# Kernel optimization log

Measured on AMD Instinct MI355X. Metric: run time of the kernel, lower is better.

## Reference

```python
import jax, jax.numpy as jnp
import numpy as np

# Production-scale dims
B, S, D = 8, 2048, 1024          # batch, seq_len, d_model
E, ES, V = 32, 128, 1024         # n_experts, expert_size, v_dim (= d_model)
K = 4                            # top-k experts per token (n_heads)


def setup_inputs() -> dict:
    key = jax.random.key(0)
    k1, k2, k3, k4 = jax.random.split(key, 4)
    return {
        "x": jax.random.normal(k1, (B, S, D), jnp.float32),
        "keys": jax.random.normal(k2, (E, D, ES), jnp.float32) * (D ** -0.5),
        "values": jax.random.normal(k3, (E, ES, V), jnp.float32) * (ES ** -0.5),
        "expert_sel": jax.random.normal(k4, (E, D), jnp.float32) * (D ** -0.5),
    }


def reference(x, keys, values, expert_sel):
    """SigmaMoELayer forward (eval mode, sigmoid selection, no bias/dropout).
    Returns (out [B,S,V], reg_loss scalar)."""
    n_experts = expert_sel.shape[0]
    # Router logits: [B, S, E]
    sel_raw = jnp.einsum('bsd,ed->bse', x, expert_sel)

    # Entropy regularization: log_softmax over experts, log-mean over all tokens
    l = jax.nn.log_softmax(sel_raw.reshape(-1, n_experts), axis=-1)   # [T, E]
    lm = jax.scipy.special.logsumexp(l, axis=0) - jnp.log(jnp.asarray(l.shape[0], l.dtype))
    reg_loss = jnp.sum(lm * jnp.exp(lm))  # == -entropy_l(lm).mean()

    # Sigmoid gating + top-k expert selection
    sel = jax.nn.sigmoid(sel_raw)
    sel_val, sel_idx = jax.lax.top_k(sel, K)                          # [B,S,K]

    # Scatter gate values onto the expert axis: gate[b,s,e] = sel_val if e selected else 0
    gate = jnp.einsum('bske,bsk->bse',
                      jax.nn.one_hot(sel_idx, n_experts, dtype=x.dtype), sel_val)

    # Expert up-projection + ReLU, gated (relu(mask*z) == mask*relu(z), experts distinct)
    h = jax.nn.relu(jnp.einsum('bsd,edf->bsef', x, keys)) * gate[..., None]  # [B,S,E,ES]
    # Expert down-projection + combine across experts
    out = jnp.einsum('bsef,efv->bsv', h, values)                      # [B,S,V]
    return out, reg_loss
```

## Files before the change

kernel.cpp:

```cpp
#include <hip/hip_runtime.h>

typedef unsigned int uint;
typedef unsigned short ushort;

#define TT 16384
#define DD 1024
#define EE 32
#define ESS 128
#define VV 1024
#define KK 4
#define TILE 64
#define NTILE_MAX 1056
#define RSPLIT 8

typedef __attribute__((ext_vector_type(8))) short bf16x8;
typedef __attribute__((ext_vector_type(16))) float f32x16;

#define WS_SELRAW   0
#define WS_GATES    524288
#define WS_PGATE    589824
#define WS_STATS    655360
#define WS_LMSUMS   655360
#define WS_COUNTS   655392
#define WS_OFFSETS  655424
#define WS_CURSORS  655457
#define WS_NTILES   655489
#define WS_TMAPE    655490
#define WS_TMAPT    656546
#define WS_IDXS     657602
#define WS_PERM     723138
#define WS_XB       788736
#define WS_KF       9177344
#define WS_VF       11274496
#define WS_ISLOT    13371648
#define WS_STG      13437184
#define WS_NEED_U   46991616ull

__device__ __forceinline__ ushort f2b(float f) {
    uint u = __builtin_bit_cast(uint, f);
    u = (u + 0x7fffu + ((u >> 16) & 1u)) >> 16;
    return (ushort)u;
}
__device__ __forceinline__ uint bpack(float lo, float hi) {
    return (uint)f2b(lo) | ((uint)f2b(hi) << 16);
}
__device__ __forceinline__ float b2f(ushort b) {
    uint u = (uint)b << 16;
    return __builtin_bit_cast(float, u);
}

__device__ __forceinline__ void gload_lds16(const void* g, void* l) {
    __builtin_amdgcn_global_load_lds(
        (const __attribute__((address_space(1))) uint*)g,
        (__attribute__((address_space(3))) uint*)l, 16, 0, 0);
}

__global__ __launch_bounds__(256) void k_prep_k(const float* __restrict__ keys,
                                                ushort* __restrict__ kfb) {
    const int e = blockIdx.x >> 6, ks = blockIdx.x & 63;
    const int nf = threadIdx.x >> 6, l = threadIdx.x & 63;
    const int f = nf * 32 + (l & 31);
    const int d0 = ks * 16 + (l >> 5) * 8;
    const float* src = keys + ((size_t)e * DD + d0) * ESS + f;
    float v[8];
#pragma unroll
    for (int j = 0; j < 8; j++) v[j] = src[(size_t)j * ESS];
    uint4 r = { bpack(v[0], v[1]), bpack(v[2], v[3]), bpack(v[4], v[5]), bpack(v[6], v[7]) };
    const size_t off = (((size_t)e * 64 + ks) * 4 + nf) * 512 + l * 8;
    *(uint4*)(kfb + off) = r;
}

__global__ __launch_bounds__(512) void k_prep_v(const float* __restrict__ values,
                                                ushort* __restrict__ vfb) {
    const int e = blockIdx.x >> 5, nv = blockIdx.x & 31;
    const int ks = threadIdx.x >> 6, l = threadIdx.x & 63;
    const int v0 = nv * 32 + (l & 31);
    const int f0 = ks * 16 + (l >> 5) * 8;
    const float* src = values + ((size_t)e * ESS + f0) * VV + v0;
    float v[8];
#pragma unroll
    for (int j = 0; j < 8; j++) v[j] = src[(size_t)j * VV];
    uint4 r = { bpack(v[0], v[1]), bpack(v[2], v[3]), bpack(v[4], v[5]), bpack(v[6], v[7]) };
    const size_t off = (((size_t)e * 32 + nv) * 8 + ks) * 512 + l * 8;
    *(uint4*)(vfb + off) = r;
}

__global__ __launch_bounds__(256) void k_router(const float* __restrict__ x,
                                                const float* __restrict__ sel,
                                                float* __restrict__ sel_part,
                                                uint* __restrict__ xbu) {
    __shared__ float xs[64][68];
    __shared__ float ss[32][68];
    const int tid = threadIdx.x;
    const int t0 = blockIdx.x * 64;
    const int dch = blockIdx.y;
    const int el = tid & 31;
    const int tg = tid >> 5;
    float acc[8];
#pragma unroll
    for (int i = 0; i < 8; i++) acc[i] = 0.f;

    const int dlen = DD / RSPLIT;
    for (int dc = dch * dlen; dc < dch * dlen + dlen; dc += 64) {
#pragma unroll
        for (int i = 0; i < 4; i++) {
            int q = tid + 256 * i;
            int r = q >> 4, c4 = q & 15;
            size_t gi = (size_t)(t0 + r) * DD + dc + c4 * 4;
            float4 v = *(const float4*)&x[gi];
            *(float4*)&xs[r][c4 * 4] = v;
            uint2 bv = { bpack(v.x, v.y), bpack(v.z, v.w) };
            *(uint2*)&xbu[gi / 2] = bv;
        }
#pragma unroll
        for (int i = 0; i < 2; i++) {
            int q = tid + 256 * i;
            int e = q >> 4, c4 = q & 15;
            float4 v = *(const float4*)&sel[(size_t)e * DD + dc + c4 * 4];
            *(float4*)&ss[e][c4 * 4] = v;
        }
        __syncthreads();
#pragma unroll
        for (int d4 = 0; d4 < 16; d4++) {
            float4 sv = *(const float4*)&ss[el][d4 * 4];
#pragma unroll
            for (int i = 0; i < 8; i++) {
                float4 xv = *(const float4*)&xs[tg * 8 + i][d4 * 4];
                acc[i] += xv.x * sv.x + xv.y * sv.y + xv.z * sv.z + xv.w * sv.w;
            }
        }
        __syncthreads();
    }
    float* dst = sel_part + (size_t)dch * TT * EE;
#pragma unroll
    for (int i = 0; i < 8; i++)
        dst[(size_t)(t0 + tg * 8 + i) * EE + el] = acc[i];
}

__global__ __launch_bounds__(256) void k_token(const float* __restrict__ sel_part,
                                               float* __restrict__ gates,
                                               int* __restrict__ idxs,
                                               float* __restrict__ lm_sums,
                                               int* __restrict__ counts) {
    __shared__ int hist[EE];
    __shared__ float lmh[EE];
    const int tid = threadIdx.x;
    if (tid < EE) { hist[tid] = 0; lmh[tid] = 0.f; }
    __syncthreads();

    const int t = blockIdx.x * 256 + tid;
    float v[32];
#pragma unroll
    for (int j = 0; j < 8; j++) {
        float4 q[RSPLIT];
#pragma unroll
        for (int p = 0; p < RSPLIT; p++)
            q[p] = *(const float4*)&sel_part[((size_t)p * TT + t) * EE + j * 4];
        v[j * 4 + 0] = ((q[0].x + q[1].x) + (q[2].x + q[3].x)) + ((q[4].x + q[5].x) + (q[6].x + q[7].x));
        v[j * 4 + 1] = ((q[0].y + q[1].y) + (q[2].y + q[3].y)) + ((q[4].y + q[5].y) + (q[6].y + q[7].y));
        v[j * 4 + 2] = ((q[0].z + q[1].z) + (q[2].z + q[3].z)) + ((q[4].z + q[5].z) + (q[6].z + q[7].z));
        v[j * 4 + 3] = ((q[0].w + q[1].w) + (q[2].w + q[3].w)) + ((q[4].w + q[5].w) + (q[6].w + q[7].w));
    }
    float m = v[0];
#pragma unroll
    for (int e = 1; e < 32; e++) m = fmaxf(m, v[e]);
    float s = 0.f;
#pragma unroll
    for (int e = 0; e < 32; e++) s += expf(v[e] - m);
    const float lse = logf(s) + m;

    float sg[32];
#pragma unroll
    for (int e = 0; e < 32; e++) sg[e] = 1.f / (1.f + expf(-v[e]));

    unsigned taken = 0u;
#pragma unroll
    for (int k = 0; k < KK; k++) {
        float best = -1.f; int bi = 0;
#pragma unroll
        for (int e = 0; e < 32; e++) {
            bool free_e = !((taken >> e) & 1u);
            if (free_e && sg[e] > best) { best = sg[e]; bi = e; }
        }
        taken |= 1u << bi;
        gates[t * KK + k] = best;
        idxs[t * KK + k] = bi;
        atomicAdd(&hist[bi], 1);
    }

#pragma unroll
    for (int e = 0; e < 32; e++) {
        float pv = expf(v[e] - lse);
#pragma unroll
        for (int o = 32; o >= 1; o >>= 1) pv += __shfl_xor(pv, o, 64);
        if ((tid & 63) == 0) atomicAdd(&lmh[e], pv);
    }
    __syncthreads();
    if (tid < EE) {
        atomicAdd(&counts[tid], hist[tid]);
        atomicAdd(&lm_sums[tid], lmh[tid]);
    }
}

__global__ void k_scan(const int* __restrict__ counts, int* __restrict__ offsets,
                       int* __restrict__ cursors, int* __restrict__ tmape,
                       int* __restrict__ tmapt, int* __restrict__ ntiles,
                       const float* __restrict__ lm_sums, float* __restrict__ out_reg) {
    const int lane = threadIdx.x;
    int c = (lane < EE) ? counts[lane] : 0;
    int p = c;
#pragma unroll
    for (int o = 1; o < 32; o <<= 1) { int u = __shfl_up(p, o, 64); if (lane >= o) p += u; }
    const int off = p - c;
    if (lane < EE) { offsets[lane] = off; cursors[lane] = off; }
    if (lane == EE - 1) offsets[EE] = p;

    int nt = (c + TILE - 1) / TILE;
    int q = nt;
#pragma unroll
    for (int o = 1; o < 32; o <<= 1) { int u = __shfl_up(q, o, 64); if (lane >= o) q += u; }
    const int tb = q - nt;
    if (lane < EE)
        for (int j = 0; j < nt; j++) { tmape[tb + j] = lane; tmapt[tb + j] = j; }
    if (lane == EE - 1) ntiles[0] = q;

    float rv = 0.f;
    if (lane < EE) {
        float pe = lm_sums[lane] * (1.f / (float)TT);
        rv = pe * logf(pe);
    }
#pragma unroll
    for (int o = 16; o >= 1; o >>= 1) rv += __shfl_down(rv, o, 64);
    if (lane == 0) out_reg[0] = rv;
}

__global__ __launch_bounds__(256) void k_scatter(const int* __restrict__ idxs,
                                                 const float* __restrict__ gates,
                                                 int* __restrict__ cursors,
                                                 int* __restrict__ perm,
                                                 float* __restrict__ pgate,
                                                 int* __restrict__ islot) {
    __shared__ int lh[EE];
    __shared__ int lbase[EE];
    const int tid = threadIdx.x;
    if (tid < EE) lh[tid] = 0;
    __syncthreads();
    const int t = blockIdx.x * 256 + tid;
    int ee[KK], rk[KK];
#pragma unroll
    for (int k = 0; k < KK; k++) {
        ee[k] = idxs[t * KK + k];
        rk[k] = atomicAdd(&lh[ee[k]], 1);
    }
    __syncthreads();
    if (tid < EE) lbase[tid] = atomicAdd(&cursors[tid], lh[tid]);
    __syncthreads();
#pragma unroll
    for (int k = 0; k < KK; k++) {
        int pos = lbase[ee[k]] + rk[k];
        perm[pos] = t;
        pgate[pos] = gates[t * KK + k];
        islot[t * KK + k] = pos;
    }
}

template <bool STG>
__global__ __launch_bounds__(256, 3) void k_expert(
    const ushort* __restrict__ xb, const ushort* __restrict__ kfb,
    const ushort* __restrict__ vfb,
    const int* __restrict__ perm, const float* __restrict__ pgate,
    const int* __restrict__ offsets, const int* __restrict__ counts,
    const int* __restrict__ tmape, const int* __restrict__ tmapt,
    const int* __restrict__ ntiles, ushort* __restrict__ stg,
    float* __restrict__ out)
{
    __shared__ __align__(1024) char xsb[2][64 * 256];
    __shared__ __align__(16) ushort hs[64][128];
    __shared__ float gl[64];
    __shared__ int tl[64];

    const int bid = (blockIdx.x & 7) * 132 + (blockIdx.x >> 3);
    if (bid >= ntiles[0]) return;
    const int e = tmape[bid];
    const int base = offsets[e] + tmapt[bid] * TILE;
    const int nr = min(TILE, offsets[e] + counts[e] - base);
    const int tid = threadIdx.x;

    if (tid < 64) {
        int tok = 0; float g = 0.f;
        if (tid < nr) { tok = perm[base + tid]; g = pgate[base + tid]; }
        tl[tid] = tok; gl[tid] = g;
    }
    __syncthreads();

    const int lane = tid & 63, wid = tid >> 6;
    const int wm = wid >> 1, wn = wid & 1;
    const int l31 = lane & 31, l5 = lane >> 5;

    const char* xbytes = (const char*)xb;
    const ushort* kb = kfb + ((size_t)e * 256 + wn * 2) * 512 + lane * 8;

    int srow[4]; const char* ssrc[4];
#pragma unroll
    for (int i = 0; i < 4; i++) {
        srow[i] = wid * 4096 + i * 1024;
        int row = wid * 16 + i * 4 + (lane >> 4);
        int colb = (lane & 15) * 16;
        ssrc[i] = xbytes + (size_t)tl[row] * 2048 + (colb ^ ((row & 15) << 4));
    }

    f32x16 acc0, acc1;
#pragma unroll
    for (int r = 0; r < 16; r++) { acc0[r] = 0.f; acc1[r] = 0.f; }

#pragma unroll
    for (int i = 0; i < 4; i++)
        gload_lds16(ssrc[i], xsb[0] + srow[i]);

    bf16x8 b0p[8], b1p[8];
#pragma unroll
    for (int j = 0; j < 8; j++) {
        b0p[j] = *(const bf16x8*)(kb + (size_t)j * 2048);
        b1p[j] = *(const bf16x8*)(kb + (size_t)j * 2048 + 512);
    }
    asm volatile("s_waitcnt vmcnt(16)" ::: "memory");
    __builtin_amdgcn_s_barrier();
    __builtin_amdgcn_sched_barrier(0);

    const int hr = wm * 32 + l31;
    const int asw = (hr & 15) << 4;

    for (int c = 0; c < 8; c++) {
        const int cur = c & 1;
        if (c < 7) {
#pragma unroll
            for (int i = 0; i < 4; i++)
                gload_lds16(ssrc[i] + (c + 1) * 256, xsb[cur ^ 1] + srow[i]);
        }
        const char* xcur = xsb[cur];
#pragma unroll
        for (int ksl = 0; ksl < 8; ksl++) {
            bf16x8 a = *(const bf16x8*)(xcur + hr * 256 + ((ksl * 32 + l5 * 16) ^ asw));
            int ks = c * 8 + ksl;
            acc0 = __builtin_amdgcn_mfma_f32_32x32x16_bf16(a, b0p[ksl], acc0, 0, 0, 0);
            acc1 = __builtin_amdgcn_mfma_f32_32x32x16_bf16(a, b1p[ksl], acc1, 0, 0, 0);
            int nk = (ks + 8) & 63;
            b0p[ksl] = *(const bf16x8*)(kb + (size_t)nk * 2048);
            b1p[ksl] = *(const bf16x8*)(kb + (size_t)nk * 2048 + 512);
        }
        asm volatile("s_waitcnt vmcnt(16)" ::: "memory");
        __builtin_amdgcn_s_barrier();
        __builtin_amdgcn_sched_barrier(0);
    }

#pragma unroll
    for (int r = 0; r < 16; r++) {
        int row = (r & 3) + 8 * (r >> 2) + 4 * l5;
        int grow = wm * 32 + row;
        float g = gl[grow];
        int c0 = wn * 64 + l31;
        int c1 = c0 + 32;
        int sw = (grow & 7) << 3;
        hs[grow][c0 ^ sw] = f2b(fmaxf(acc0[r], 0.f) * g);
        hs[grow][c1 ^ sw] = f2b(fmaxf(acc1[r], 0.f) * g);
    }
    __syncthreads();

    bf16x8 af[8];
    const int hsw = (hr & 7) << 3;
#pragma unroll
    for (int ks = 0; ks < 8; ks++) {
        int cc = ks * 16 + l5 * 8;
        af[ks] = *(const bf16x8*)&hs[hr][cc ^ hsw];
    }

    const ushort* vb = vfb + ((size_t)e * 32 + wn * 16) * 4096 + lane * 8;
    bf16x8 vpa[4], vpb[4];
#pragma unroll
    for (int j = 0; j < 4; j++) {
        vpa[j] = *(const bf16x8*)(vb + (size_t)j * 512);
        vpb[j] = *(const bf16x8*)(vb + (size_t)(4 + j) * 512);
    }

#pragma unroll
    for (int nv = 0; nv < 16; nv++) {
        f32x16 acc;
#pragma unroll
        for (int r = 0; r < 16; r++) acc[r] = 0.f;
#pragma unroll
        for (int ks = 0; ks < 4; ks++)
            acc = __builtin_amdgcn_mfma_f32_32x32x16_bf16(af[ks], vpa[ks], acc, 0, 0, 0);
        if (nv < 15) {
#pragma unroll
            for (int j = 0; j < 4; j++)
                vpa[j] = *(const bf16x8*)(vb + ((size_t)(nv + 1) * 8 + j) * 512);
        }
#pragma unroll
        for (int ks = 0; ks < 4; ks++)
            acc = __builtin_amdgcn_mfma_f32_32x32x16_bf16(af[4 + ks], vpb[ks], acc, 0, 0, 0);
        if (nv < 15) {
#pragma unroll
            for (int j = 0; j < 4; j++)
                vpb[j] = *(const bf16x8*)(vb + ((size_t)(nv + 1) * 8 + 4 + j) * 512);
        }
        const int colb = wn * 512 + nv * 32 + l31;
#pragma unroll
        for (int r = 0; r < 16; r++) {
            int row = wm * 32 + (r & 3) + 8 * (r >> 2) + 4 * l5;
            if (row < nr) {
                if (STG)
                    stg[(size_t)(base + row) * VV + colb] = f2b(acc[r]);
                else
                    atomicAdd(&out[(size_t)tl[row] * VV + colb], acc[r]);
            }
        }
    }
}

__global__ __launch_bounds__(256) void k_combine(const ushort* __restrict__ stg,
                                                 const int* __restrict__ islot,
                                                 float* __restrict__ out) {
    const int tid = threadIdx.x;
    const int t = blockIdx.x * 2 + (tid >> 7);
    const int c8 = (tid & 127) * 8;
    const int4 sl = *(const int4*)&islot[t * KK];
    float acc[8];
#pragma unroll
    for (int j = 0; j < 8; j++) acc[j] = 0.f;
    const int slots[4] = { sl.x, sl.y, sl.z, sl.w };
#pragma unroll
    for (int k = 0; k < KK; k++) {
        bf16x8 v = *(const bf16x8*)(stg + (size_t)slots[k] * VV + c8);
#pragma unroll
        for (int j = 0; j < 8; j++) acc[j] += b2f((ushort)v[j]);
    }
    float4 o0 = { acc[0], acc[1], acc[2], acc[3] };
    float4 o1 = { acc[4], acc[5], acc[6], acc[7] };
    *(float4*)&out[(size_t)t * VV + c8] = o0;
    *(float4*)&out[(size_t)t * VV + c8 + 4] = o1;
}

extern "C" void kernel_launch(void* const* d_in, const int* in_sizes, int n_in,
                              void* d_out, int out_size, void* d_ws, size_t ws_size,
                              hipStream_t stream) {
    const float* x      = (const float*)d_in[0];
    const float* keys   = (const float*)d_in[1];
    const float* values = (const float*)d_in[2];
    const float* esel   = (const float*)d_in[3];
    float* out = (float*)d_out;

    float* wsf = (float*)d_ws;
    int*   wsi = (int*)d_ws;

    float* gates   = wsf + WS_GATES;
    float* pgate   = wsf + WS_PGATE;
    float* lm_sums = wsf + WS_LMSUMS;
    int*   counts  = wsi + WS_COUNTS;
    int*   offsets = wsi + WS_OFFSETS;
    int*   cursors = wsi + WS_CURSORS;
    int*   ntiles  = wsi + WS_NTILES;
    int*   tmape   = wsi + WS_TMAPE;
    int*   tmapt   = wsi + WS_TMAPT;
    int*   idxs    = wsi + WS_IDXS;
    int*   perm    = wsi + WS_PERM;
    int*   islot   = wsi + WS_ISLOT;
    uint*   xbu = (uint*)(wsf + WS_XB);
    ushort* xb  = (ushort*)xbu;
    ushort* kfb = (ushort*)(wsf + WS_KF);
    ushort* vfb = (ushort*)(wsf + WS_VF);
    ushort* stg = (ushort*)(wsf + WS_STG);

    const bool use_stg = ws_size >= WS_NEED_U * 4ull;
    float* sel_part = use_stg ? (float*)stg : (float*)kfb;

    if (!use_stg)
        hipMemsetAsync(d_out, 0, (size_t)TT * VV * sizeof(float), stream);
    hipMemsetAsync(wsf + WS_STATS, 0, 64 * sizeof(float), stream);

    k_router<<<dim3(TT / 64, RSPLIT), 256, 0, stream>>>(x, esel, sel_part, xbu);
    k_token<<<TT / 256, 256, 0, stream>>>(sel_part, gates, idxs, lm_sums, counts);

    k_prep_k<<<EE * 64, 256, 0, stream>>>(keys, kfb);
    k_prep_v<<<EE * 32, 512, 0, stream>>>(values, vfb);

    k_scan<<<1, 64, 0, stream>>>(counts, offsets, cursors, tmape, tmapt, ntiles,
                                 lm_sums, out + (size_t)TT * VV);
    k_scatter<<<TT / 256, 256, 0, stream>>>(idxs, gates, cursors, perm, pgate, islot);
    if (use_stg) {
        k_expert<true><<<NTILE_MAX, 256, 0, stream>>>(xb, kfb, vfb, perm, pgate,
                                                      offsets, counts, tmape, tmapt,
                                                      ntiles, stg, out);
        k_combine<<<TT / 2, 256, 0, stream>>>(stg, islot, out);
    } else {
        k_expert<false><<<NTILE_MAX, 256, 0, stream>>>(xb, kfb, vfb, perm, pgate,
                                                       offsets, counts, tmape, tmapt,
                                                       ntiles, stg, out);
    }
}
```

Measured before the change: 212.3 us.

## Repartition expert GEMM waves to split only along N, reusing B fragments across M

Each of the four waves previously owned a 32-row by 64-column quadrant of the 64x128 hidden tile and of the output. Now each wave covers all 64 token rows and a quarter of the columns, in both the up-projection and the down-projection. Every key and value fragment loaded from global memory now feeds two MFMAs (one per 32-row half), which halves per-wave weight traffic and prefetch register use. In exchange, each wave makes twice as many LDS reads of activation rows.

Result: slower. 278.3 us (+31.1%).

```diff
diff --git a/kernel.cpp b/kernel.cpp
--- a/kernel.cpp
+++ b/kernel.cpp
@@ -294,11 +294,11 @@
     __syncthreads();
 
     const int lane = tid & 63, wid = tid >> 6;
-    const int wm = wid >> 1, wn = wid & 1;
+    const int wn = wid;
     const int l31 = lane & 31, l5 = lane >> 5;
 
     const char* xbytes = (const char*)xb;
-    const ushort* kb = kfb + ((size_t)e * 256 + wn * 2) * 512 + lane * 8;
+    const ushort* kb = kfb + ((size_t)e * 256 + wn) * 512 + lane * 8;
 
     int srow[4]; const char* ssrc[4];
 #pragma unroll
@@ -317,18 +317,15 @@
     for (int i = 0; i < 4; i++)
         gload_lds16(ssrc[i], xsb[0] + srow[i]);
 
-    bf16x8 b0p[8], b1p[8];
-#pragma unroll
-    for (int j = 0; j < 8; j++) {
-        b0p[j] = *(const bf16x8*)(kb + (size_t)j * 2048);
-        b1p[j] = *(const bf16x8*)(kb + (size_t)j * 2048 + 512);
-    }
-    asm volatile("s_waitcnt vmcnt(16)" ::: "memory");
+    bf16x8 bp[8];
+#pragma unroll
+    for (int j = 0; j < 8; j++)
+        bp[j] = *(const bf16x8*)(kb + (size_t)j * 2048);
+    asm volatile("s_waitcnt vmcnt(8)" ::: "memory");
     __builtin_amdgcn_s_barrier();
     __builtin_amdgcn_sched_barrier(0);
 
-    const int hr = wm * 32 + l31;
-    const int asw = (hr & 15) << 4;
+    const int asw = (l31 & 15) << 4;
 
     for (int c = 0; c < 8; c++) {
         const int cur = c & 1;
@@ -340,78 +337,71 @@
         const char* xcur = xsb[cur];
 #pragma unroll
         for (int ksl = 0; ksl < 8; ksl++) {
-            bf16x8 a = *(const bf16x8*)(xcur + hr * 256 + ((ksl * 32 + l5 * 16) ^ asw));
+            int co = (ksl * 32 + l5 * 16) ^ asw;
+            bf16x8 a0 = *(const bf16x8*)(xcur + l31 * 256 + co);
+            bf16x8 a1 = *(const bf16x8*)(xcur + (32 + l31) * 256 + co);
             int ks = c * 8 + ksl;
-            acc0 = __builtin_amdgcn_mfma_f32_32x32x16_bf16(a, b0p[ksl], acc0, 0, 0, 0);
-            acc1 = __builtin_amdgcn_mfma_f32_32x32x16_bf16(a, b1p[ksl], acc1, 0, 0, 0);
+            acc0 = __builtin_amdgcn_mfma_f32_32x32x16_bf16(a0, bp[ksl], acc0, 0, 0, 0);
+            acc1 = __builtin_amdgcn_mfma_f32_32x32x16_bf16(a1, bp[ksl], acc1, 0, 0, 0);
             int nk = (ks + 8) & 63;
-            b0p[ksl] = *(const bf16x8*)(kb + (size_t)nk * 2048);
-            b1p[ksl] = *(const bf16x8*)(kb + (size_t)nk * 2048 + 512);
-        }
-        asm volatile("s_waitcnt vmcnt(16)" ::: "memory");
+            bp[ksl] = *(const bf16x8*)(kb + (size_t)nk * 2048);
+        }
+        asm volatile("s_waitcnt vmcnt(8)" ::: "memory");
         __builtin_amdgcn_s_barrier();
         __builtin_amdgcn_sched_barrier(0);
     }
 
 #pragma unroll
     for (int r = 0; r < 16; r++) {
-        int row = (r & 3) + 8 * (r >> 2) + 4 * l5;
-        int grow = wm * 32 + row;
-        float g = gl[grow];
-        int c0 = wn * 64 + l31;
-        int c1 = c0 + 32;
-        int sw = (grow & 7) << 3;
-        hs[grow][c0 ^ sw] = f2b(fmaxf(acc0[r], 0.f) * g);
-        hs[grow][c1 ^ sw] = f2b(fmaxf(acc1[r], 0.f) * g);
-    }
-    __syncthreads();
-
-    bf16x8 af[8];
-    const int hsw = (hr & 7) << 3;
-#pragma unroll
-    for (int ks = 0; ks < 8; ks++) {
-        int cc = ks * 16 + l5 * 8;
-        af[ks] = *(const bf16x8*)&hs[hr][cc ^ hsw];
-    }
-
-    const ushort* vb = vfb + ((size_t)e * 32 + wn * 16) * 4096 + lane * 8;
-    bf16x8 vpa[4], vpb[4];
-#pragma unroll
-    for (int j = 0; j < 4; j++) {
-        vpa[j] = *(const bf16x8*)(vb + (size_t)j * 512);
-        vpb[j] = *(const bf16x8*)(vb + (size_t)(4 + j) * 512);
-    }
-
-#pragma unroll
-    for (int nv = 0; nv < 16; nv++) {
-        f32x16 acc;
-#pragma unroll
-        for (int r = 0; r < 16; r++) acc[r] = 0.f;
-#pragma unroll
-        for (int ks = 0; ks < 4; ks++)
-            acc = __builtin_amdgcn_mfma_f32_32x32x16_bf16(af[ks], vpa[ks], acc, 0, 0, 0);
-        if (nv < 15) {
-#pragma unroll
-            for (int j = 0; j < 4; j++)
-                vpa[j] = *(const bf16x8*)(vb + ((size_t)(nv + 1) * 8 + j) * 512);
-        }
-#pragma unroll
-        for (int ks = 0; ks < 4; ks++)
-            acc = __builtin_amdgcn_mfma_f32_32x32x16_bf16(af[4 + ks], vpb[ks], acc, 0, 0, 0);
-        if (nv < 15) {
-#pragma unroll
-            for (int j = 0; j < 4; j++)
-                vpb[j] = *(const bf16x8*)(vb + ((size_t)(nv + 1) * 8 + 4 + j) * 512);
-        }
-        const int colb = wn * 512 + nv * 32 + l31;
+        int row0 = (r & 3) + 8 * (r >> 2) + 4 * l5;
+        int row1 = row0 + 32;
+        int cc = wn * 32 + l31;
+        hs[row0][cc ^ ((row0 & 7) << 3)] = f2b(fmaxf(acc0[r], 0.f) * gl[row0]);
+        hs[row1][cc ^ ((row1 & 7) << 3)] = f2b(fmaxf(acc1[r], 0.f) * gl[row1]);
+    }
+    __syncthreads();
+
+    bf16x8 af[2][8];
+#pragma unroll
+    for (int b = 0; b < 2; b++) {
+        int hr2 = b * 32 + l31;
+        int hsw = (hr2 & 7) << 3;
+#pragma unroll
+        for (int ks = 0; ks < 8; ks++)
+            af[b][ks] = *(const bf16x8*)&hs[hr2][(ks * 16 + l5 * 8) ^ hsw];
+    }
+
+    const ushort* vb = vfb + ((size_t)e * 32 + wn * 8) * 4096 + lane * 8;
+    bf16x8 vp[8];
+#pragma unroll
+    for (int ks = 0; ks < 8; ks++)
+        vp[ks] = *(const bf16x8*)(vb + (size_t)ks * 512);
+
+#pragma unroll
+    for (int j = 0; j < 8; j++) {
+        f32x16 o0, o1;
+#pragma unroll
+        for (int r = 0; r < 16; r++) { o0[r] = 0.f; o1[r] = 0.f; }
+#pragma unroll
+        for (int ks = 0; ks < 8; ks++) {
+            bf16x8 v = vp[ks];
+            o0 = __builtin_amdgcn_mfma_f32_32x32x16_bf16(af[0][ks], v, o0, 0, 0, 0);
+            o1 = __builtin_amdgcn_mfma_f32_32x32x16_bf16(af[1][ks], v, o1, 0, 0, 0);
+            if (j < 7)
+                vp[ks] = *(const bf16x8*)(vb + ((size_t)(j + 1) * 8 + ks) * 512);
+        }
+        const int colb = wn * 256 + j * 32 + l31;
 #pragma unroll
         for (int r = 0; r < 16; r++) {
-            int row = wm * 32 + (r & 3) + 8 * (r >> 2) + 4 * l5;
-            if (row < nr) {
-                if (STG)
-                    stg[(size_t)(base + row) * VV + colb] = f2b(acc[r]);
-                else
-                    atomicAdd(&out[(size_t)tl[row] * VV + colb], acc[r]);
+            int row0 = (r & 3) + 8 * (r >> 2) + 4 * l5;
+            int row1 = row0 + 32;
+            if (row0 < nr) {
+                if (STG) stg[(size_t)(base + row0) * VV + colb] = f2b(o0[r]);
+                else     atomicAdd(&out[(size_t)tl[row0] * VV + colb], o0[r]);
+            }
+            if (row1 < nr) {
+                if (STG) stg[(size_t)(base + row1) * VV + colb] = f2b(o1[r]);
+                else     atomicAdd(&out[(size_t)tl[row1] * VV + colb], o1[r]);
             }
         }
     }
```
